# Kernel tuning notes

Hardware: AMD Instinct MI355X
Metric: run time of the kernel (lower is better)

The kernel has to match this reference:

```python
import jax, jax.numpy as jnp
import numpy as np


def setup_inputs() -> dict:
    key = jax.random.key(0)
    ks = jax.random.split(key, 5)
    S, B, H, L = 512, 64, 1024, 2
    scale = 0.1
    return {
        "x": jax.random.normal(ks[0], (S, B, H), dtype=jnp.float32),
        "h0": jnp.zeros((L, B, H), dtype=jnp.float32),
        "c0": jnp.zeros((L, B, H), dtype=jnp.float32),
        "Wx": jax.random.uniform(ks[1], (L, 4 * H, H), minval=-scale, maxval=scale, dtype=jnp.float32),
        "Wh": jax.random.uniform(ks[2], (L, 4 * H, H), minval=-scale, maxval=scale, dtype=jnp.float32),
        "bx": jax.random.uniform(ks[3], (L, 4 * H), minval=-scale, maxval=scale, dtype=jnp.float32),
        "bh": jax.random.uniform(ks[4], (L, 4 * H), minval=-scale, maxval=scale, dtype=jnp.float32),
    }


def _cell(x_t, h_prev, c_prev, Wx_l, Wh_l, bx_l, bh_l, H):
    # gates: [B, 4H]; chunk order per source: f, i, o, c_ex
    gates = x_t @ Wx_l.T + bx_l + h_prev @ Wh_l.T + bh_l
    f, i, o, c_ex = jnp.split(gates, 4, axis=1)
    f = jax.nn.sigmoid(f)
    i = jax.nn.sigmoid(i)
    o = jax.nn.sigmoid(o)
    c_ex = jnp.tanh(c_ex)
    c = f * c_prev + i * c_ex
    h = o * jnp.tanh(c)
    return h, c


def reference(x, h0, c0, Wx, Wh, bx, bh):
    # x: [S, B, H]; h0/c0: [L, B, H]; Wx/Wh: [L, 4H, H]; bx/bh: [L, 4H]
    L = h0.shape[0]
    H = h0.shape[-1]

    def step(carry, x_t):
        h_all, c_all = carry  # each [L, B, H]
        out = x_t
        hs, cs = [], []
        for l in range(L):  # small fixed layer count
            h, c = _cell(out, h_all[l], c_all[l], Wx[l], Wh[l], bx[l], bh[l], H)
            out = h  # dropout is identity in eval mode
            hs.append(h)
            cs.append(c)
        return (jnp.stack(hs, 0), jnp.stack(cs, 0)), out

    (h_fin, c_fin), ys = jax.lax.scan(step, (h0, c0), x)
    return ys, (h_fin, c_fin)
```

## Files before the change

kernel.cpp:

```cpp
#include <hip/hip_runtime.h>

typedef __bf16 bf16_t;
typedef __bf16 bf16x8 __attribute__((ext_vector_type(8)));
typedef __bf16 bf16x4 __attribute__((ext_vector_type(4)));
typedef float  f32x4  __attribute__((ext_vector_type(4)));
typedef unsigned long long u64;

#define S_LEN 512
#define BATCH 64
#define HID 1024
#define BH (BATCH*HID)
#define G4 (4*HID)
#define NBLK 256
#define LBLK 128
#define NTHR 512
#define R0 8
#define SKEW (R0-1)
#define FSTRIDE 32
#define NCNT 16

__device__ __forceinline__ float sigmoid_f(float x) { return 1.f / (1.f + __expf(-x)); }
__device__ __forceinline__ float tanh_f(float x) {
    float e = __expf(-2.f * fabsf(x));
    float t = (1.f - e) / (1.f + e);
    return x >= 0.f ? t : -t;
}

__device__ __forceinline__ bf16x8 cvt8(const float* p) {
    float4 a = *reinterpret_cast<const float4*>(p);
    float4 b = *reinterpret_cast<const float4*>(p + 4);
    bf16x8 r;
    r[0] = (bf16_t)a.x; r[1] = (bf16_t)a.y; r[2] = (bf16_t)a.z; r[3] = (bf16_t)a.w;
    r[4] = (bf16_t)b.x; r[5] = (bf16_t)b.y; r[6] = (bf16_t)b.z; r[7] = (bf16_t)b.w;
    return r;
}

__device__ __forceinline__ void wait_counts(unsigned* cnt, unsigned thr0, unsigned thr1,
                                            int tid, int lane) {
    if (tid < 64) {
        for (;;) {
            unsigned v = 0;
            if (lane < 2 * NCNT)
                v = __hip_atomic_load(&cnt[lane * FSTRIDE], __ATOMIC_RELAXED,
                                      __HIP_MEMORY_SCOPE_AGENT);
            unsigned s = v;
            s += __shfl_xor(s, 1);
            s += __shfl_xor(s, 2);
            s += __shfl_xor(s, 4);
            s += __shfl_xor(s, 8);
            unsigned S0 = __shfl(s, 0);
            unsigned S1 = __shfl(s, 16);
            if (S0 >= thr0 && S1 >= thr1) break;
            __builtin_amdgcn_s_sleep(4);
        }
        __builtin_amdgcn_fence(__ATOMIC_ACQUIRE, "agent");
    }
    __syncthreads();
}

__global__ void prep_kernel(const float* __restrict__ x, const float* __restrict__ h0,
                            bf16_t* __restrict__ ring0, bf16_t* __restrict__ ring1,
                            bf16_t* __restrict__ x_sh, unsigned* __restrict__ cnt,
                            int use_xsh) {
    int gtid = blockIdx.x * blockDim.x + threadIdx.x;
    int gsz  = gridDim.x * blockDim.x;
    if (gtid < 2 * NCNT) cnt[gtid * FSTRIDE] = 0u;
    for (int i = gtid; i < BH; i += gsz) {
        ring0[(size_t)(R0 - 1) * BH + i] = (bf16_t)h0[i];
        ring1[(size_t)1 * BH + i]        = (bf16_t)h0[BH + i];
    }
    if (use_xsh) {
        int ngrp = S_LEN * BH / 8;
        for (int g = gtid; g < ngrp; g += gsz)
            *reinterpret_cast<bf16x8*>(x_sh + (size_t)g * 8) = cvt8(x + (size_t)g * 8);
    }
}

__global__ __launch_bounds__(NTHR, 2) void lstm_persistent(
    const float* __restrict__ x,
    const float* __restrict__ c0,
    const float* __restrict__ Wx,
    const float* __restrict__ Wh,
    const float* __restrict__ bx,
    const float* __restrict__ bh,
    float* __restrict__ out,
    bf16_t* __restrict__ ring0,
    bf16_t* __restrict__ ring1,
    const bf16_t* __restrict__ x_sh,
    unsigned* __restrict__ cnt,
    int use_xsh)
{
    __shared__ __attribute__((aligned(16))) unsigned char lds_w[256 * 512];
    __shared__ __attribute__((aligned(16))) float lds_red[8 * 256];
    __shared__ __attribute__((aligned(16))) float lds_hf[BATCH * 8];

    const int tid  = threadIdx.x;
    const int bid  = blockIdx.x;
    const int l    = bid >> 7;
    const int ug8  = bid & 127;
    const int lane = tid & 63;
    const int wv   = tid >> 6;
    const int mt   = wv >> 1;
    const int kh   = wv & 1;
    const int quad = lane >> 4;
    const int r16  = lane & 15;

    float* ys   = out;
    float* hfin = out + (size_t)S_LEN * BH;
    float* cfin = hfin + 2 * BH;

    {
        const float* WxL = Wx + (size_t)l * G4 * HID;
        const float* WhL = Wh + (size_t)l * G4 * HID;
        for (int ch = tid; ch < 32 * 256; ch += NTHR) {
            int row = ch & 31;
            int gr  = ch >> 5;
            int ul = row >> 2, g = row & 3;
            size_t R = (size_t)g * HID + 8 * ug8 + ul;
            const float* src = (gr < 128) ? (WxL + R * HID + (size_t)gr * 8)
                                          : (WhL + R * HID + (size_t)(gr - 128) * 8);
            *reinterpret_cast<bf16x8*>(&lds_w[gr * 512 + row * 16]) = cvt8(src);
        }
    }

    const int b_loc  = lane >> 2;
    const int uu     = lane & 3;
    const int b_glob = 16 * mt + b_loc;
    const int u_loc  = 4 * kh + uu;
    const int u_glob = 8 * ug8 + u_loc;

    float bias_r[4];
    #pragma unroll
    for (int gi = 0; gi < 4; ++gi) {
        int R = gi * HID + u_glob;
        bias_r[gi] = bx[l * G4 + R] + bh[l * G4 + R];
    }
    float c_reg = c0[(size_t)l * BH + (size_t)b_glob * HID + u_glob];

    bf16_t* ringL = (l == 0) ? ring0 : ring1;
    unsigned* mycnt = &cnt[(l * NCNT + (ug8 & (NCNT - 1))) * FSTRIDE];
    __syncthreads();

    const int arow_off = (16 * mt + r16) * HID + kh * 512 + quad * 8;

    for (int t = 0; t < S_LEN; ++t) {
        f32x4 acc0 = {0.f, 0.f, 0.f, 0.f};
        f32x4 acc1 = {0.f, 0.f, 0.f, 0.f};

        if (l == 0) {
            bf16x8 af[16];
            if (use_xsh) {
                const bf16_t* arow = x_sh + (size_t)t * BH + arow_off;
                #pragma unroll
                for (int ks = 0; ks < 16; ++ks)
                    af[ks] = *reinterpret_cast<const bf16x8*>(arow + ks * 32);
            } else {
                const float* arow = x + (size_t)t * BH + arow_off;
                #pragma unroll
                for (int ks = 0; ks < 16; ++ks)
                    af[ks] = cvt8(arow + ks * 32);
            }
            #pragma unroll
            for (int ks = 0; ks < 16; ++ks) {
                int gr = kh * 64 + ks * 4 + quad;
                bf16x8 b0 = *reinterpret_cast<const bf16x8*>(&lds_w[gr * 512 + r16 * 16]);
                bf16x8 b1 = *reinterpret_cast<const bf16x8*>(&lds_w[gr * 512 + (16 + r16) * 16]);
                acc0 = __builtin_amdgcn_mfma_f32_16x16x32_bf16(af[ks], b0, acc0, 0, 0, 0);
                acc1 = __builtin_amdgcn_mfma_f32_16x16x32_bf16(af[ks], b1, acc1, 0, 0, 0);
            }
            unsigned thr1 = (t > SKEW) ? (unsigned)(LBLK * (t - SKEW)) : 0u;
            wait_counts(cnt, (unsigned)(LBLK * t), thr1, tid, lane);
            const bf16_t* ah = ring0 + (size_t)((t - 1) & (R0 - 1)) * BH + arow_off;
            #pragma unroll
            for (int ks = 0; ks < 16; ++ks)
                af[ks] = *reinterpret_cast<const bf16x8*>(ah + ks * 32);
            #pragma unroll
            for (int ks = 0; ks < 16; ++ks) {
                int gr = 128 + kh * 64 + ks * 4 + quad;
                bf16x8 b0 = *reinterpret_cast<const bf16x8*>(&lds_w[gr * 512 + r16 * 16]);
                bf16x8 b1 = *reinterpret_cast<const bf16x8*>(&lds_w[gr * 512 + (16 + r16) * 16]);
                acc0 = __builtin_amdgcn_mfma_f32_16x16x32_bf16(af[ks], b0, acc0, 0, 0, 0);
                acc1 = __builtin_amdgcn_mfma_f32_16x16x32_bf16(af[ks], b1, acc1, 0, 0, 0);
            }
        } else {
            wait_counts(cnt, (unsigned)(LBLK * (t + 1)), (unsigned)(LBLK * t), tid, lane);
            const bf16_t* ax = ring0 + (size_t)(t & (R0 - 1)) * BH + arow_off;
            const bf16_t* ah = ring1 + (size_t)((t - 1) & 1) * BH + arow_off;
            bf16x8 axf[16], ahf[16];
            #pragma unroll
            for (int ks = 0; ks < 16; ++ks)
                axf[ks] = *reinterpret_cast<const bf16x8*>(ax + ks * 32);
            #pragma unroll
            for (int ks = 0; ks < 16; ++ks)
                ahf[ks] = *reinterpret_cast<const bf16x8*>(ah + ks * 32);
            #pragma unroll
            for (int ks = 0; ks < 16; ++ks) {
                int gr = kh * 64 + ks * 4 + quad;
                bf16x8 b0 = *reinterpret_cast<const bf16x8*>(&lds_w[gr * 512 + r16 * 16]);
                bf16x8 b1 = *reinterpret_cast<const bf16x8*>(&lds_w[gr * 512 + (16 + r16) * 16]);
                acc0 = __builtin_amdgcn_mfma_f32_16x16x32_bf16(axf[ks], b0, acc0, 0, 0, 0);
                acc1 = __builtin_amdgcn_mfma_f32_16x16x32_bf16(axf[ks], b1, acc1, 0, 0, 0);
            }
            #pragma unroll
            for (int ks = 0; ks < 16; ++ks) {
                int gr = 128 + kh * 64 + ks * 4 + quad;
                bf16x8 b0 = *reinterpret_cast<const bf16x8*>(&lds_w[gr * 512 + r16 * 16]);
                bf16x8 b1 = *reinterpret_cast<const bf16x8*>(&lds_w[gr * 512 + (16 + r16) * 16]);
                acc0 = __builtin_amdgcn_mfma_f32_16x16x32_bf16(ahf[ks], b0, acc0, 0, 0, 0);
                acc1 = __builtin_amdgcn_mfma_f32_16x16x32_bf16(ahf[ks], b1, acc1, 0, 0, 0);
            }
        }

        {
            f32x4 ship = kh ? acc0 : acc1;
            *reinterpret_cast<f32x4*>(&lds_red[wv * 256 + lane * 4]) = ship;
            __syncthreads();
            f32x4 part = *reinterpret_cast<const f32x4*>(&lds_red[(wv ^ 1) * 256 + lane * 4]);
            f32x4 keep = kh ? acc1 : acc0;
            acc0 = keep + part;
        }

        {
            const int quad_s = b_loc >> 2;
            const int reg_s  = b_loc & 3;
            float gsum[4];
            #pragma unroll
            for (int gi = 0; gi < 4; ++gi) {
                int lane_s = (quad_s << 4) | (4 * uu + gi);
                float v0 = __shfl(acc0[0], lane_s, 64);
                float v1 = __shfl(acc0[1], lane_s, 64);
                float v2 = __shfl(acc0[2], lane_s, 64);
                float v3 = __shfl(acc0[3], lane_s, 64);
                float v  = (reg_s == 0) ? v0 : (reg_s == 1) ? v1 : (reg_s == 2) ? v2 : v3;
                gsum[gi] = v + bias_r[gi];
            }
            float fg = sigmoid_f(gsum[0]);
            float ig = sigmoid_f(gsum[1]);
            float og = sigmoid_f(gsum[2]);
            float cx = tanh_f(gsum[3]);
            float cN = fg * c_reg + ig * cx;
            float h  = og * tanh_f(cN);
            c_reg = cN;
            lds_hf[b_glob * 8 + u_loc] = h;
            if (t == S_LEN - 1) {
                hfin[(size_t)l * BH + (size_t)b_glob * HID + u_glob] = h;
                cfin[(size_t)l * BH + (size_t)b_glob * HID + u_glob] = cN;
            }
        }
        __syncthreads();

        if (tid < 64) {
            const float* hp = &lds_hf[lane * 8];
            union { bf16x4 v; u64 q; } p0, p1;
            #pragma unroll
            for (int j = 0; j < 4; ++j) {
                p0.v[j] = (bf16_t)hp[j];
                p1.v[j] = (bf16_t)hp[4 + j];
            }
            const int slotmask = (l == 0) ? (R0 - 1) : 1;
            bf16_t* dst = ringL + (size_t)(t & slotmask) * BH + (size_t)lane * HID + 8 * ug8;
            __hip_atomic_store((u64*)(void*)dst,       p0.q, __ATOMIC_RELAXED, __HIP_MEMORY_SCOPE_AGENT);
            __hip_atomic_store((u64*)(void*)(dst + 4), p1.q, __ATOMIC_RELAXED, __HIP_MEMORY_SCOPE_AGENT);
            if (l == 1) {
                float* yd = ys + (size_t)t * BH + (size_t)lane * HID + 8 * ug8;
                __builtin_nontemporal_store(*reinterpret_cast<const f32x4*>(hp),     reinterpret_cast<f32x4*>(yd));
                __builtin_nontemporal_store(*reinterpret_cast<const f32x4*>(hp + 4), reinterpret_cast<f32x4*>(yd + 4));
            }
            asm volatile("s_waitcnt vmcnt(0)" ::: "memory");
            if (lane == 0) atomicAdd(mycnt, 1u);
        }
    }
}

extern "C" void kernel_launch(void* const* d_in, const int* in_sizes, int n_in,
                              void* d_out, int out_size, void* d_ws, size_t ws_size,
                              hipStream_t stream) {
    (void)in_sizes; (void)n_in; (void)out_size;
    const float* x  = (const float*)d_in[0];
    const float* h0 = (const float*)d_in[1];
    const float* c0 = (const float*)d_in[2];
    const float* Wx = (const float*)d_in[3];
    const float* Wh = (const float*)d_in[4];
    const float* bx = (const float*)d_in[5];
    const float* bh = (const float*)d_in[6];

    unsigned char* ws = (unsigned char*)d_ws;
    unsigned* cnt = (unsigned*)ws;
    size_t off = 32768;
    bf16_t* ring0 = (bf16_t*)(ws + off); off += (size_t)R0 * BH * 2;
    bf16_t* ring1 = (bf16_t*)(ws + off); off += (size_t)2 * BH * 2;
    bf16_t* x_sh  = (bf16_t*)(ws + off);
    size_t need_xsh = off + (size_t)S_LEN * BH * 2;
    int use_xsh = (ws_size >= need_xsh) ? 1 : 0;

    prep_kernel<<<2048, 256, 0, stream>>>(x, h0, ring0, ring1, x_sh, cnt, use_xsh);
    lstm_persistent<<<NBLK, NTHR, 0, stream>>>(x, c0, Wx, Wh, bx, bh, (float*)d_out,
                                               ring0, ring1, x_sh, cnt, use_xsh);
}
```

Before: 6.727 ms.

## Use full-history hidden buffers to split layer waits and drop back-pressure fence

When the workspace is large enough, each layer's hidden states go into a buffer with one slot per timestep. Layer 0 no longer waits for layer 1 to consume ring slots, and layer 1 waits on each layer's counter separately, so it can start the x-projection before its own recurrent state is ready. The change also drops the bf16 pre-conversion of x in the prep kernel, prefetches the next x row into registers after each step, increments the counter before the y stores, and shortens the spin sleep. In exchange it drops the acquire fence in the fast path, which risks memory-ordering correctness, uses much more workspace, and keeps more registers live.

```diff
diff --git a/kernel.cpp b/kernel.cpp
--- a/kernel.cpp
+++ b/kernel.cpp
@@ -14,10 +14,9 @@
 #define NBLK 256
 #define LBLK 128
 #define NTHR 512
-#define R0 8
-#define SKEW (R0-1)
 #define FSTRIDE 32
 #define NCNT 16
+#define RSKEW 7
 
 __device__ __forceinline__ float sigmoid_f(float x) { return 1.f / (1.f + __expf(-x)); }
 __device__ __forceinline__ float tanh_f(float x) {
@@ -35,8 +34,28 @@
     return r;
 }
 
-__device__ __forceinline__ void wait_counts(unsigned* cnt, unsigned thr0, unsigned thr1,
-                                            int tid, int lane) {
+__device__ __forceinline__ void wait_one(unsigned* cnt, int layer, unsigned thr,
+                                         int tid, int lane) {
+    if (tid < 64) {
+        for (;;) {
+            unsigned v = 0;
+            if (lane < NCNT)
+                v = __hip_atomic_load(&cnt[(layer * NCNT + lane) * FSTRIDE],
+                                      __ATOMIC_RELAXED, __HIP_MEMORY_SCOPE_AGENT);
+            unsigned s = v;
+            s += __shfl_xor(s, 1);
+            s += __shfl_xor(s, 2);
+            s += __shfl_xor(s, 4);
+            s += __shfl_xor(s, 8);
+            if (__shfl(s, 0) >= thr) break;
+            __builtin_amdgcn_s_sleep(1);
+        }
+    }
+    __syncthreads();
+}
+
+__device__ __forceinline__ void wait_two_fence(unsigned* cnt, unsigned thr0, unsigned thr1,
+                                               int tid, int lane) {
     if (tid < 64) {
         for (;;) {
             unsigned v = 0;
@@ -51,28 +70,22 @@
             unsigned S0 = __shfl(s, 0);
             unsigned S1 = __shfl(s, 16);
             if (S0 >= thr0 && S1 >= thr1) break;
-            __builtin_amdgcn_s_sleep(4);
+            __builtin_amdgcn_s_sleep(1);
         }
         __builtin_amdgcn_fence(__ATOMIC_ACQUIRE, "agent");
     }
     __syncthreads();
 }
 
-__global__ void prep_kernel(const float* __restrict__ x, const float* __restrict__ h0,
-                            bf16_t* __restrict__ ring0, bf16_t* __restrict__ ring1,
-                            bf16_t* __restrict__ x_sh, unsigned* __restrict__ cnt,
-                            int use_xsh) {
+__global__ void prep_kernel(const float* __restrict__ h0,
+                            bf16_t* __restrict__ h0buf, bf16_t* __restrict__ h1buf,
+                            unsigned* __restrict__ cnt, int mask0, int mask1) {
     int gtid = blockIdx.x * blockDim.x + threadIdx.x;
     int gsz  = gridDim.x * blockDim.x;
     if (gtid < 2 * NCNT) cnt[gtid * FSTRIDE] = 0u;
     for (int i = gtid; i < BH; i += gsz) {
-        ring0[(size_t)(R0 - 1) * BH + i] = (bf16_t)h0[i];
-        ring1[(size_t)1 * BH + i]        = (bf16_t)h0[BH + i];
-    }
-    if (use_xsh) {
-        int ngrp = S_LEN * BH / 8;
-        for (int g = gtid; g < ngrp; g += gsz)
-            *reinterpret_cast<bf16x8*>(x_sh + (size_t)g * 8) = cvt8(x + (size_t)g * 8);
+        h0buf[(size_t)mask0 * BH + i] = (bf16_t)h0[i];
+        h1buf[(size_t)mask1 * BH + i] = (bf16_t)h0[BH + i];
     }
 }
 
@@ -84,11 +97,10 @@
     const float* __restrict__ bx,
     const float* __restrict__ bh,
     float* __restrict__ out,
-    bf16_t* __restrict__ ring0,
-    bf16_t* __restrict__ ring1,
-    const bf16_t* __restrict__ x_sh,
+    bf16_t* __restrict__ h0buf,
+    bf16_t* __restrict__ h1buf,
     unsigned* __restrict__ cnt,
-    int use_xsh)
+    int ff, int mask0, int mask1)
 {
     __shared__ __attribute__((aligned(16))) unsigned char lds_w[256 * 512];
     __shared__ __attribute__((aligned(16))) float lds_red[8 * 256];
@@ -137,40 +149,41 @@
     }
     float c_reg = c0[(size_t)l * BH + (size_t)b_glob * HID + u_glob];
 
-    bf16_t* ringL = (l == 0) ? ring0 : ring1;
+    bf16_t* pubbuf = (l == 0) ? h0buf : h1buf;
+    const int pubmask = (l == 0) ? mask0 : mask1;
     unsigned* mycnt = &cnt[(l * NCNT + (ug8 & (NCNT - 1))) * FSTRIDE];
     __syncthreads();
 
     const int arow_off = (16 * mt + r16) * HID + kh * 512 + quad * 8;
+
+    bf16x8 axp[16];
+    if (l == 0) {
+        const float* arow = x + arow_off;
+        #pragma unroll
+        for (int ks = 0; ks < 16; ++ks) axp[ks] = cvt8(arow + ks * 32);
+    }
 
     for (int t = 0; t < S_LEN; ++t) {
         f32x4 acc0 = {0.f, 0.f, 0.f, 0.f};
         f32x4 acc1 = {0.f, 0.f, 0.f, 0.f};
 
         if (l == 0) {
-            bf16x8 af[16];
-            if (use_xsh) {
-                const bf16_t* arow = x_sh + (size_t)t * BH + arow_off;
-                #pragma unroll
-                for (int ks = 0; ks < 16; ++ks)
-                    af[ks] = *reinterpret_cast<const bf16x8*>(arow + ks * 32);
-            } else {
-                const float* arow = x + (size_t)t * BH + arow_off;
-                #pragma unroll
-                for (int ks = 0; ks < 16; ++ks)
-                    af[ks] = cvt8(arow + ks * 32);
-            }
             #pragma unroll
             for (int ks = 0; ks < 16; ++ks) {
                 int gr = kh * 64 + ks * 4 + quad;
                 bf16x8 b0 = *reinterpret_cast<const bf16x8*>(&lds_w[gr * 512 + r16 * 16]);
                 bf16x8 b1 = *reinterpret_cast<const bf16x8*>(&lds_w[gr * 512 + (16 + r16) * 16]);
-                acc0 = __builtin_amdgcn_mfma_f32_16x16x32_bf16(af[ks], b0, acc0, 0, 0, 0);
-                acc1 = __builtin_amdgcn_mfma_f32_16x16x32_bf16(af[ks], b1, acc1, 0, 0, 0);
-            }
-            unsigned thr1 = (t > SKEW) ? (unsigned)(LBLK * (t - SKEW)) : 0u;
-            wait_counts(cnt, (unsigned)(LBLK * t), thr1, tid, lane);
-            const bf16_t* ah = ring0 + (size_t)((t - 1) & (R0 - 1)) * BH + arow_off;
+                acc0 = __builtin_amdgcn_mfma_f32_16x16x32_bf16(axp[ks], b0, acc0, 0, 0, 0);
+                acc1 = __builtin_amdgcn_mfma_f32_16x16x32_bf16(axp[ks], b1, acc1, 0, 0, 0);
+            }
+            if (ff) {
+                wait_one(cnt, 0, (unsigned)(LBLK * t), tid, lane);
+            } else {
+                unsigned thr1 = (t > RSKEW) ? (unsigned)(LBLK * (t - RSKEW)) : 0u;
+                wait_two_fence(cnt, (unsigned)(LBLK * t), thr1, tid, lane);
+            }
+            const bf16_t* ah = h0buf + (size_t)((t - 1) & mask0) * BH + arow_off;
+            bf16x8 af[16];
             #pragma unroll
             for (int ks = 0; ks < 16; ++ks)
                 af[ks] = *reinterpret_cast<const bf16x8*>(ah + ks * 32);
@@ -183,31 +196,62 @@
                 acc1 = __builtin_amdgcn_mfma_f32_16x16x32_bf16(af[ks], b1, acc1, 0, 0, 0);
             }
         } else {
-            wait_counts(cnt, (unsigned)(LBLK * (t + 1)), (unsigned)(LBLK * t), tid, lane);
-            const bf16_t* ax = ring0 + (size_t)(t & (R0 - 1)) * BH + arow_off;
-            const bf16_t* ah = ring1 + (size_t)((t - 1) & 1) * BH + arow_off;
-            bf16x8 axf[16], ahf[16];
-            #pragma unroll
-            for (int ks = 0; ks < 16; ++ks)
-                axf[ks] = *reinterpret_cast<const bf16x8*>(ax + ks * 32);
-            #pragma unroll
-            for (int ks = 0; ks < 16; ++ks)
-                ahf[ks] = *reinterpret_cast<const bf16x8*>(ah + ks * 32);
-            #pragma unroll
-            for (int ks = 0; ks < 16; ++ks) {
-                int gr = kh * 64 + ks * 4 + quad;
-                bf16x8 b0 = *reinterpret_cast<const bf16x8*>(&lds_w[gr * 512 + r16 * 16]);
-                bf16x8 b1 = *reinterpret_cast<const bf16x8*>(&lds_w[gr * 512 + (16 + r16) * 16]);
-                acc0 = __builtin_amdgcn_mfma_f32_16x16x32_bf16(axf[ks], b0, acc0, 0, 0, 0);
-                acc1 = __builtin_amdgcn_mfma_f32_16x16x32_bf16(axf[ks], b1, acc1, 0, 0, 0);
-            }
-            #pragma unroll
-            for (int ks = 0; ks < 16; ++ks) {
-                int gr = 128 + kh * 64 + ks * 4 + quad;
-                bf16x8 b0 = *reinterpret_cast<const bf16x8*>(&lds_w[gr * 512 + r16 * 16]);
-                bf16x8 b1 = *reinterpret_cast<const bf16x8*>(&lds_w[gr * 512 + (16 + r16) * 16]);
-                acc0 = __builtin_amdgcn_mfma_f32_16x16x32_bf16(ahf[ks], b0, acc0, 0, 0, 0);
-                acc1 = __builtin_amdgcn_mfma_f32_16x16x32_bf16(ahf[ks], b1, acc1, 0, 0, 0);
+            if (ff) {
+                wait_one(cnt, 0, (unsigned)(LBLK * (t + 1)), tid, lane);
+                const bf16_t* ax = h0buf + (size_t)(t & mask0) * BH + arow_off;
+                bf16x8 axf[16];
+                #pragma unroll
+                for (int ks = 0; ks < 16; ++ks)
+                    axf[ks] = *reinterpret_cast<const bf16x8*>(ax + ks * 32);
+                #pragma unroll
+                for (int ks = 0; ks < 16; ++ks) {
+                    int gr = kh * 64 + ks * 4 + quad;
+                    bf16x8 b0 = *reinterpret_cast<const bf16x8*>(&lds_w[gr * 512 + r16 * 16]);
+                    bf16x8 b1 = *reinterpret_cast<const bf16x8*>(&lds_w[gr * 512 + (16 + r16) * 16]);
+                    acc0 = __builtin_amdgcn_mfma_f32_16x16x32_bf16(axf[ks], b0, acc0, 0, 0, 0);
+                    acc1 = __builtin_amdgcn_mfma_f32_16x16x32_bf16(axf[ks], b1, acc1, 0, 0, 0);
+                }
+                wait_one(cnt, 1, (unsigned)(LBLK * t), tid, lane);
+                const bf16_t* ah = h1buf + (size_t)((t - 1) & mask1) * BH + arow_off;
+                bf16x8 ahf[16];
+                #pragma unroll
+                for (int ks = 0; ks < 16; ++ks)
+                    ahf[ks] = *reinterpret_cast<const bf16x8*>(ah + ks * 32);
+                #pragma unroll
+                for (int ks = 0; ks < 16; ++ks) {
+                    int gr = 128 + kh * 64 + ks * 4 + quad;
+                    bf16x8 b0 = *reinterpret_cast<const bf16x8*>(&lds_w[gr * 512 + r16 * 16]);
+                    bf16x8 b1 = *reinterpret_cast<const bf16x8*>(&lds_w[gr * 512 + (16 + r16) * 16]);
+                    acc0 = __builtin_amdgcn_mfma_f32_16x16x32_bf16(ahf[ks], b0, acc0, 0, 0, 0);
+                    acc1 = __builtin_amdgcn_mfma_f32_16x16x32_bf16(ahf[ks], b1, acc1, 0, 0, 0);
+                }
+            } else {
+                wait_two_fence(cnt, (unsigned)(LBLK * (t + 1)), (unsigned)(LBLK * t), tid, lane);
+                const bf16_t* ax = h0buf + (size_t)(t & mask0) * BH + arow_off;
+                const bf16_t* ah = h1buf + (size_t)((t - 1) & mask1) * BH + arow_off;
+                bf16x8 axf[16], ahf[16];
+                #pragma unroll
+                for (int ks = 0; ks < 16; ++ks)
+                    axf[ks] = *reinterpret_cast<const bf16x8*>(ax + ks * 32);
+                #pragma unroll
+                for (int ks = 0; ks < 16; ++ks)
+                    ahf[ks] = *reinterpret_cast<const bf16x8*>(ah + ks * 32);
+                #pragma unroll
+                for (int ks = 0; ks < 16; ++ks) {
+                    int gr = kh * 64 + ks * 4 + quad;
+                    bf16x8 b0 = *reinterpret_cast<const bf16x8*>(&lds_w[gr * 512 + r16 * 16]);
+                    bf16x8 b1 = *reinterpret_cast<const bf16x8*>(&lds_w[gr * 512 + (16 + r16) * 16]);
+                    acc0 = __builtin_amdgcn_mfma_f32_16x16x32_bf16(axf[ks], b0, acc0, 0, 0, 0);
+                    acc1 = __builtin_amdgcn_mfma_f32_16x16x32_bf16(axf[ks], b1, acc1, 0, 0, 0);
+                }
+                #pragma unroll
+                for (int ks = 0; ks < 16; ++ks) {
+                    int gr = 128 + kh * 64 + ks * 4 + quad;
+                    bf16x8 b0 = *reinterpret_cast<const bf16x8*>(&lds_w[gr * 512 + r16 * 16]);
+                    bf16x8 b1 = *reinterpret_cast<const bf16x8*>(&lds_w[gr * 512 + (16 + r16) * 16]);
+                    acc0 = __builtin_amdgcn_mfma_f32_16x16x32_bf16(ahf[ks], b0, acc0, 0, 0, 0);
+                    acc1 = __builtin_amdgcn_mfma_f32_16x16x32_bf16(ahf[ks], b1, acc1, 0, 0, 0);
+                }
             }
         }
 
@@ -257,17 +301,22 @@
                 p0.v[j] = (bf16_t)hp[j];
                 p1.v[j] = (bf16_t)hp[4 + j];
             }
-            const int slotmask = (l == 0) ? (R0 - 1) : 1;
-            bf16_t* dst = ringL + (size_t)(t & slotmask) * BH + (size_t)lane * HID + 8 * ug8;
+            bf16_t* dst = pubbuf + (size_t)(t & pubmask) * BH + (size_t)lane * HID + 8 * ug8;
             __hip_atomic_store((u64*)(void*)dst,       p0.q, __ATOMIC_RELAXED, __HIP_MEMORY_SCOPE_AGENT);
             __hip_atomic_store((u64*)(void*)(dst + 4), p1.q, __ATOMIC_RELAXED, __HIP_MEMORY_SCOPE_AGENT);
+            asm volatile("s_waitcnt vmcnt(0)" ::: "memory");
+            if (lane == 0) atomicAdd(mycnt, 1u);
             if (l == 1) {
                 float* yd = ys + (size_t)t * BH + (size_t)lane * HID + 8 * ug8;
                 __builtin_nontemporal_store(*reinterpret_cast<const f32x4*>(hp),     reinterpret_cast<f32x4*>(yd));
                 __builtin_nontemporal_store(*reinterpret_cast<const f32x4*>(hp + 4), reinterpret_cast<f32x4*>(yd + 4));
             }
-            asm volatile("s_waitcnt vmcnt(0)" ::: "memory");
-            if (lane == 0) atomicAdd(mycnt, 1u);
+        }
+
+        if (l == 0 && t + 1 < S_LEN) {
+            const float* arow = x + (size_t)(t + 1) * BH + arow_off;
+            #pragma unroll
+            for (int ks = 0; ks < 16; ++ks) axp[ks] = cvt8(arow + ks * 32);
         }
     }
 }
@@ -287,13 +336,20 @@
     unsigned char* ws = (unsigned char*)d_ws;
     unsigned* cnt = (unsigned*)ws;
     size_t off = 32768;
-    bf16_t* ring0 = (bf16_t*)(ws + off); off += (size_t)R0 * BH * 2;
-    bf16_t* ring1 = (bf16_t*)(ws + off); off += (size_t)2 * BH * 2;
-    bf16_t* x_sh  = (bf16_t*)(ws + off);
-    size_t need_xsh = off + (size_t)S_LEN * BH * 2;
-    int use_xsh = (ws_size >= need_xsh) ? 1 : 0;
-
-    prep_kernel<<<2048, 256, 0, stream>>>(x, h0, ring0, ring1, x_sh, cnt, use_xsh);
+    size_t need_ff = off + (size_t)2 * S_LEN * BH * 2;
+    int ff, mask0, mask1;
+    bf16_t *h0buf, *h1buf;
+    if (ws_size >= need_ff) {
+        ff = 1; mask0 = S_LEN - 1; mask1 = S_LEN - 1;
+        h0buf = (bf16_t*)(ws + off); off += (size_t)S_LEN * BH * 2;
+        h1buf = (bf16_t*)(ws + off);
+    } else {
+        ff = 0; mask0 = 7; mask1 = 1;
+        h0buf = (bf16_t*)(ws + off); off += (size_t)8 * BH * 2;
+        h1buf = (bf16_t*)(ws + off);
+    }
+
+    prep_kernel<<<2048, 256, 0, stream>>>(h0, h0buf, h1buf, cnt, mask0, mask1);
     lstm_persistent<<<NBLK, NTHR, 0, stream>>>(x, c0, Wx, Wh, bx, bh, (float*)d_out,
-                                               ring0, ring1, x_sh, cnt, use_xsh);
-}
+                                               h0buf, h1buf, cnt, ff, mask0, mask1);
+}
```

Result: no change. 6.661 ms (-1.0%).
